# Optimization experiments

Hardware: AMD Instinct MI355X
Metric: run time of the kernel (lower is better)

## Reference

```python
import jax, jax.numpy as jnp
import numpy as np

N = 512       # nodes
V = 8         # n_vectors_hidden
F = 128       # n_invariant_feat_hidden
H = 8         # num_heads
BESSEL = 8
R_MAX = 10.0
FH = F // H
VH = V // H

def _edges(n):
    s, r = np.meshgrid(np.arange(n), np.arange(n), indexing='ij')
    m = s != r
    return jnp.asarray(s[m], jnp.int32), jnp.asarray(r[m], jnp.int32)

def _sph(v):
    # real spherical harmonics ell=1,2,3, e3nn 'component' normalization, unit input v[...,3] -> [...,15]
    x, y, z = v[..., 0], v[..., 1], v[..., 2]
    s3, s15, s5 = np.sqrt(3.0), np.sqrt(15.0), np.sqrt(5.0)
    sh1 = jnp.stack([x, y, z], -1) * s3
    sh2 = jnp.stack([s15 * x * y, s15 * y * z, 0.5 * s5 * (3 * z**2 - 1), s15 * x * z, 0.5 * s15 * (x**2 - y**2)], -1)
    c33, c32, c31, c30 = np.sqrt(35.0 / 8.0), np.sqrt(105.0), np.sqrt(21.0 / 8.0), 0.5 * np.sqrt(7.0)
    sh3 = jnp.stack([c33 * y * (3 * x**2 - y**2), c32 * x * y * z, c31 * y * (5 * z**2 - 1), c30 * z * (5 * z**2 - 3), c31 * x * (5 * z**2 - 1), 0.5 * c32 * z * (x**2 - y**2), c33 * x * (x**2 - 3 * y**2)], -1)
    return jnp.concatenate([sh1, sh2, sh3], -1)

def _bessel(x, n, x_max):
    # e3nn.bessel basis: sqrt(2/x_max) * sin(k*pi*x/x_max) / x, k=1..n
    x = x[..., None]
    k = jnp.arange(1, n + 1, dtype=x.dtype)
    x_safe = jnp.where(x == 0, 1.0, x)
    return np.sqrt(2.0 / x_max) * jnp.sin(k * jnp.pi * x / x_max) / x_safe

def _sus(x):
    return jnp.where(x > 0, jnp.exp(-1.0 / jnp.where(x > 0, x, 1.0)), 0.0)

def _soft_envelope(x, x_max, a=2.0, v0=1.2):
    return v0 * _sus(a * (1.0 - x / x_max)) / _sus(jnp.asarray(a, x.dtype))

def _forward(positions, features, We0, be0, We1, be1, Wq, Wk, Wek, Wv, Wev, Wg, Wo0, bo0, Wo1, bo1, Wo2, bo2):
    n = positions.shape[0]
    senders, receivers = _edges(n)
    vec = positions[senders] - positions[receivers]               # [E,V,3] gather
    lengths = jnp.sqrt(jnp.sum(vec * vec, -1) + 1e-20)            # safe_norm [E,V]
    unit = vec / lengths[..., None]
    sph = _sph(unit)                                              # [E,V,15]
    radial = _bessel(lengths, BESSEL, R_MAX) * _soft_envelope(lengths, R_MAX)[..., None]  # [E,V,B]
    e_scal = radial.reshape(radial.shape[0], -1)                  # [E, V*B]
    h = jax.nn.silu(e_scal @ We0 + be0)
    h = jax.nn.silu(h @ We1 + be1)                                # edge MLP, output_activation=silu
    E = h.shape[0]
    q = (features @ Wq).reshape(n, H, FH)
    k = (features[senders] @ Wk + h @ Wek).reshape(E, H, FH)
    logits = jnp.einsum('ehf,ehf->eh', q[receivers], k) / np.sqrt(FH)
    seg_max = jax.ops.segment_max(logits, receivers, num_segments=n)
    ex = jnp.exp(logits - seg_max[receivers])                     # edge_weight_cutoff = 1
    denom = jax.ops.segment_sum(ex, receivers, num_segments=n)
    alpha = ex / denom[receivers]                                 # [E,H] per-receiver softmax
    v_s = (features[senders] @ Wv + h @ Wev).reshape(E, H, FH)
    gate = h @ Wg                                                 # [E,V] invariant gates
    v_vec = (gate[..., None] * sph[..., :3]).reshape(E, H, VH, 3) # equivariant values from ell=1 sph
    agg_s = jax.ops.segment_sum(alpha[..., None] * v_s, receivers, num_segments=n).reshape(n, F)
    agg_v = jax.ops.segment_sum(alpha[:, :, None, None] * v_vec, receivers, num_segments=n).reshape(n, V, 3)
    o = jax.nn.silu(agg_s @ Wo0 + bo0)
    o = jax.nn.silu(o @ Wo1 + bo1)
    o = o @ Wo2 + bo2                                             # hk MLP: last layer linear
    return (positions + agg_v, features + o)

def setup_inputs() -> dict:
    key = jax.random.key(0)
    ks = jax.random.split(key, 16)
    def w(k, i, o):
        return jax.random.normal(k, (i, o), jnp.float32) / np.sqrt(i)
    M = 128
    D = V * BESSEL
    return {
        'positions': jax.random.normal(ks[0], (N, V, 3), jnp.float32),
        'features': jax.random.normal(ks[1], (N, F), jnp.float32),
        'We0': w(ks[2], D, M), 'be0': jnp.zeros((M,), jnp.float32),
        'We1': w(ks[3], M, M), 'be1': jnp.zeros((M,), jnp.float32),
        'Wq': w(ks[4], F, F), 'Wk': w(ks[5], F, F), 'Wek': w(ks[6], M, F),
        'Wv': w(ks[7], F, F), 'Wev': w(ks[8], M, F), 'Wg': w(ks[9], M, V),
        'Wo0': w(ks[10], F, M), 'bo0': jnp.zeros((M,), jnp.float32),
        'Wo1': w(ks[11], M, M), 'bo1': jnp.zeros((M,), jnp.float32),
        'Wo2': w(ks[12], M, F), 'bo2': jnp.zeros((F,), jnp.float32),
    }

def reference(positions, features, We0, be0, We1, be1, Wq, Wk, Wek, Wv, Wev, Wg, Wo0, bo0, Wo1, bo1, Wo2, bo2):
    return _forward(positions, features, We0, be0, We1, be1, Wq, Wk, Wek, Wv, Wev, Wg, Wo0, bo0, Wo1, bo1, Wo2, bo2)
```

## Files before the change

kernel.cpp:

```cpp
#include <hip/hip_runtime.h>
#include <hip/hip_bf16.h>

#define WS_KNB  0
#define WS_VNT  32768
#define WS_QNB  65536
#define WS_A4T  98304
#define WS_WGT  360448
#define WS_W0T  360960
#define WS_W1T  365056
#define WS_PS   373248
#define PS_STRIDE 1072

typedef short bf16x8 __attribute__((ext_vector_type(8)));
typedef short short4v __attribute__((ext_vector_type(4)));
typedef float f32x4 __attribute__((ext_vector_type(4)));
typedef unsigned short ushort_t;

static __device__ __forceinline__ ushort_t f2b(float x) {
  __hip_bfloat16 h = __float2bfloat16(x);
  return reinterpret_cast<ushort_t&>(h);
}
static __device__ __forceinline__ float b2f(ushort_t u) {
  unsigned v = ((unsigned)u) << 16;
  return reinterpret_cast<float&>(v);
}
static __device__ __forceinline__ float fsilu(float x) {
  return x * __builtin_amdgcn_rcpf(1.f + __expf(-x));
}

static __device__ __forceinline__ bf16x8 radial_frag(
    float dx, float dy, float dz, float& ux, float& uy, float& uz)
{
  const float l2 = fmaf(dx,dx, fmaf(dy,dy, fmaf(dz,dz, 1e-20f)));
  const float inv = rsqrtf(l2);
  const float len = l2 * inv;
  ux = dx*inv; uy = dy*inv; uz = dz*inv;
  const float yy = 2.f - len*0.2f;
  const float env = (yy > 0.f) ? 1.9784655648f * __expf(-__builtin_amdgcn_rcpf(yy)) : 0.f;
  const float coef = 0.4472135955f * env * inv;
  const float arg = len * 0.31415926535f;
  const float s1v = __sinf(arg), c1v = __cosf(arg);
  const float twc = 2.f*c1v;
  float sp = 0.f, sc = s1v;
  bf16x8 ev;
#pragma unroll
  for (int bb = 0; bb < 8; ++bb) {
    ev[bb] = (short)f2b(coef*sc);
    const float nx = fmaf(twc, sc, -sp);
    sp = sc; sc = nx;
  }
  return ev;
}

__global__ __launch_bounds__(128) void k_prep(
    const float* __restrict__ feat, const float* __restrict__ Wq,
    const float* __restrict__ Wk, const float* __restrict__ Wv,
    const float* __restrict__ Wek, const float* __restrict__ Wg,
    const float* __restrict__ We0, const float* __restrict__ We1,
    float* __restrict__ ws)
{
  const int blk = blockIdx.x, j = threadIdx.x;
  if (blk >= 512) {
    const int i = (blk - 512)*128 + j;
    ushort_t* W0T = (ushort_t*)(ws + WS_W0T);
    ushort_t* W1T = (ushort_t*)(ws + WS_W1T);
    if (i < 8192) {
      const int n = i >> 6, k = i & 63;
      W0T[n*64 + k] = f2b(We0[k*128 + n]);
    } else {
      const int t = i - 8192, n = t >> 7, k = t & 127;
      W1T[n*128 + k] = f2b(We1[k*128 + n]);
    }
    return;
  }
  const int r = blk;
  __shared__ float fr[128];
  __shared__ float qL[128];
  fr[j] = feat[r*128 + j];
  __syncthreads();
  float aq = 0.f, ak = 0.f, av = 0.f;
#pragma unroll 4
  for (int i = 0; i < 128; ++i) {
    const float f = fr[i];
    aq = fmaf(f, Wq[i*128 + j], aq);
    ak = fmaf(f, Wk[i*128 + j], ak);
    av = fmaf(f, Wv[i*128 + j], av);
  }
  ushort_t* knB = (ushort_t*)(ws + WS_KNB);
  ushort_t* vnT = (ushort_t*)(ws + WS_VNT);
  ushort_t* qnB = (ushort_t*)(ws + WS_QNB);
  knB[r*128 + j] = f2b(ak);
  vnT[j*512 + r] = f2b(av);
  qnB[r*128 + j] = f2b(0.25f * aq);
  qL[j] = aq;
  __syncthreads();
  ushort_t* A4 = (ushort_t*)(ws + WS_A4T) + r*1024;
  const float* wr = Wek + j*128;
#pragma unroll
  for (int h = 0; h < 8; ++h) {
    float acc = 0.f;
#pragma unroll
    for (int f = 0; f < 16; ++f)
      acc = fmaf(wr[16*h + f], qL[16*h + f], acc);
    A4[h*128 + j] = f2b(acc * 0.25f);
  }
  if (r == 0) {
    ushort_t* WgT = (ushort_t*)(ws + WS_WGT);
#pragma unroll
    for (int v = 0; v < 8; ++v)
      WgT[v*128 + j] = f2b(Wg[j*8 + v]);
  }
}

#define MFMA(a,b,c) __builtin_amdgcn_mfma_f32_16x16x32_bf16((a),(b),(c),0,0,0)

__global__ __launch_bounds__(512, 4) void k_edge14(
    const float* __restrict__ pos,
    const float* __restrict__ be0, const float* __restrict__ be1,
    float* __restrict__ ws)
{
  __shared__ __align__(16) char Lds[40960];
  ushort_t* H1   = (ushort_t*)(Lds);
  ushort_t* Pb   = (ushort_t*)(Lds);
  float*    rscL = (float*)(Lds + 2048);
  ushort_t* H2t  = (ushort_t*)(Lds + 16384);
  ushort_t* Es   = (ushort_t*)(Lds + 32768);
  float*    lgT0 = (float*)(Lds + 32768);
  float*    lgT1 = (float*)(Lds + 36864);

  const int tid = threadIdx.x;
  const int nw = tid >> 6, l = tid & 63;
  const int c = l & 15, g = l >> 4;
  const int b = blockIdx.x;
  const int r = b >> 2, quarter = b & 3;
  const int base = quarter * 128;

  const ushort_t* knB = (const ushort_t*)(ws + WS_KNB);
  const ushort_t* vnT = (const ushort_t*)(ws + WS_VNT);
  const ushort_t* qnB = (const ushort_t*)(ws + WS_QNB);
  const ushort_t* A4G = (const ushort_t*)(ws + WS_A4T) + r*1024;
  const ushort_t* WgG = (const ushort_t*)(ws + WS_WGT);
  const ushort_t* W0T = (const ushort_t*)(ws + WS_W0T);
  const ushort_t* W1T = (const ushort_t*)(ws + WS_W1T);

  const int ncol = nw*16 + c;
  const float be0v = be0[ncol], be1v = be1[ncol];
  const int m_lg = nw & 3, kh = nw >> 2;
  const int ncswz = ((ncol & 7) ^ ((ncol >> 3) & 7)) & 7;

  const float prx = pos[r*24 + nw*3 + 0];
  const float pry = pos[r*24 + nw*3 + 1];
  const float prz = pos[r*24 + nw*3 + 2];

  f32x4 bh = {0,0,0,0}, sna = {0,0,0,0};
  float avx = 0.f, avy = 0.f, avz = 0.f;
  float mrun = -1e30f, drun = 0.f;
  float ux, uy, uz;

  {
    const int sg = base + l;
    const bf16x8 ev = radial_frag(pos[sg*24 + nw*3 + 0] - prx,
                                  pos[sg*24 + nw*3 + 1] - pry,
                                  pos[sg*24 + nw*3 + 2] - prz, ux, uy, uz);
    *(bf16x8*)(Es + l*64 + ((nw ^ (l&7))<<3)) = ev;
  }
  __syncthreads();

  for (int tile = 0; tile < 2; ++tile) {
    const int gbase = base + tile*64;

    float npx = 0.f, npy = 0.f, npz = 0.f;
    if (tile < 1) {
      const int sg = gbase + 64 + l;
      npx = pos[sg*24 + nw*3 + 0];
      npy = pos[sg*24 + nw*3 + 1];
      npz = pos[sg*24 + nw*3 + 2];
    }

    {
      const bf16x8 w0f0 = *(const bf16x8*)(W0T + ncol*64 + g*8);
      const bf16x8 w0f1 = *(const bf16x8*)(W0T + ncol*64 + 32 + g*8);
#pragma unroll
      for (int m = 0; m < 4; ++m) {
        const int ra = m*16 + c;
        const bf16x8 e0 = *(const bf16x8*)(Es + ra*64 + (((g  ) ^ (ra&7))<<3));
        const bf16x8 e1 = *(const bf16x8*)(Es + ra*64 + (((4+g) ^ (ra&7))<<3));
        f32x4 acc = {0,0,0,0};
        acc = MFMA(e0, w0f0, acc);
        acc = MFMA(e1, w0f1, acc);
#pragma unroll
        for (int i = 0; i < 4; ++i) {
          const int row = m*16 + g*4 + i;
          H1[row*128 + (((ncol>>3) ^ (row&15))<<3) + (c&7)] =
              f2b(fsilu(acc[i] + be0v));
        }
      }
    }
    __syncthreads();

#pragma unroll
    for (int m = 0; m < 4; ++m) {
      const int ra = m*16 + c;
      f32x4 acc = {0,0,0,0};
#pragma unroll
      for (int kb = 0; kb < 4; ++kb) {
        const bf16x8 af = *(const bf16x8*)(H1 + ra*128 + (((kb*4+g) ^ (ra&15))<<3));
        const bf16x8 wf = *(const bf16x8*)(W1T + ncol*128 + kb*32 + g*8);
        acc = MFMA(af, wf, acc);
      }
      short4v pk;
#pragma unroll
      for (int i = 0; i < 4; ++i)
        pk[i] = (short)f2b(fsilu(acc[i] + be1v));
      *(short4v*)(H2t + ncol*64 +
          ((((m*2 + (g>>1)) ^ ncswz) & 7)<<3) + (g&1)*4) = pk;
    }
    __syncthreads();

    {
      f32x4 lg = {0,0,0,0};
      if (kh == 0) {
        const int rb = m_lg*2 + (c>>3);
        const int rl = c & 7;
        const ushort_t* ab = (c < 8) ? (A4G + c*128) : (WgG + (c-8)*128);
#pragma unroll
        for (int kb = 0; kb < 4; ++kb) {
          const int cc = (kb*4 + g) & 7;
          bf16x8 bb;
#pragma unroll
          for (int j = 0; j < 8; ++j)
            bb[j] = (short)H2t[(kb*32 + g*8 + j)*64 +
                               (((rb ^ j ^ cc) & 7)<<3) + rl];
          const bf16x8 aw = *(const bf16x8*)(ab + kb*32 + g*8);
          lg = MFMA(aw, bb, lg);
        }
      } else {
        const int srow = gbase + m_lg*16 + c;
#pragma unroll
        for (int kb = 0; kb < 4; ++kb) {
          const bf16x8 bb = *(const bf16x8*)(knB + srow*128 + kb*32 + g*8);
          const bf16x8 qf = *(const bf16x8*)(qnB + r*128 + kb*32 + g*8);
          bf16x8 aw;
          const bool hit = (kb*2 + (g>>1)) == c;
#pragma unroll
          for (int j = 0; j < 8; ++j) aw[j] = hit ? qf[j] : (short)0;
          lg = MFMA(aw, bb, lg);
        }
      }
      float* lgW = kh ? lgT1 : lgT0;
#pragma unroll
      for (int i = 0; i < 4; ++i) {
        const int ch = g*4 + i;
        lgW[ch*64 + ((m_lg*16 + c) ^ (g<<4))] = lg[i];
      }
    }
    __syncthreads();

    {
      const int h = nw;
      const int kv = (h>>2)<<4;
      const int kg = ((8+h)>>2)<<4;
      float lgv = lgT0[h*64 + (l ^ kv)] + lgT1[h*64 + (l ^ kv)];
      const float gate = lgT0[(8+h)*64 + (l ^ kg)] + lgT1[(8+h)*64 + (l ^ kg)];
      if (gbase + l == r) lgv = -1e30f;
      float t = lgv;
      t = fmaxf(t, __shfl_xor(t, 1));
      t = fmaxf(t, __shfl_xor(t, 2));
      t = fmaxf(t, __shfl_xor(t, 4));
      t = fmaxf(t, __shfl_xor(t, 8));
      t = fmaxf(t, __shfl_xor(t, 16));
      t = fmaxf(t, __shfl_xor(t, 32));
      const float mnew = fmaxf(mrun, t);
      const float rsc = __expf(mrun - mnew);
      mrun = mnew;
      const float val = __expf(lgv - mnew);
      float wsm = val;
      wsm += __shfl_xor(wsm, 1);
      wsm += __shfl_xor(wsm, 2);
      wsm += __shfl_xor(wsm, 4);
      wsm += __shfl_xor(wsm, 8);
      wsm += __shfl_xor(wsm, 16);
      wsm += __shfl_xor(wsm, 32);
      drun = drun*rsc + wsm;
      const float ga = val * gate;
      Pb[h*64 + (((l>>3) ^ h)<<3) + (l&7)] = f2b(val);
      Pb[(8+h)*64 + (((l>>3) ^ h)<<3) + (l&7)] = f2b(ga);
      if (l == 0) rscL[h] = rsc;
      avx = avx*rsc + ga*ux;
      avy = avy*rsc + ga*uy;
      avz = avz*rsc + ga*uz;
    }
    __syncthreads();

    {
      float rs[4];
#pragma unroll
      for (int i = 0; i < 4; ++i) rs[i] = rscL[(4*g + i) & 7];
#pragma unroll
      for (int i = 0; i < 4; ++i) { bh[i] *= rs[i]; sna[i] *= rs[i]; }
      const bf16x8 pa0 = *(const bf16x8*)(Pb + c*64 + (((g  ) ^ (c&7))<<3));
      const bf16x8 pa1 = *(const bf16x8*)(Pb + c*64 + (((4+g) ^ (c&7))<<3));
      bh = MFMA(pa0, *(const bf16x8*)(H2t + ncol*64 +
               ((((g  ) ^ ncswz) & 7)<<3)), bh);
      bh = MFMA(pa1, *(const bf16x8*)(H2t + ncol*64 +
               ((((4+g) ^ ncswz) & 7)<<3)), bh);
      const bf16x8 vnf0 = *(const bf16x8*)(vnT + ncol*512 + gbase + g*8);
      const bf16x8 vnf1 = *(const bf16x8*)(vnT + ncol*512 + gbase + 32 + g*8);
      sna = MFMA(pa0, vnf0, sna);
      sna = MFMA(pa1, vnf1, sna);
    }
    if (tile < 1) {
      const bf16x8 ev = radial_frag(npx - prx, npy - pry, npz - prz, ux, uy, uz);
      *(bf16x8*)(Es + l*64 + ((nw ^ (l&7))<<3)) = ev;
      __syncthreads();
    }
  }

  float* PSf = ws + WS_PS + b*PS_STRIDE;
  ushort_t* PSs = (ushort_t*)PSf;
  if (g < 2) {
#pragma unroll
    for (int i = 0; i < 4; ++i) {
      PSs[(4*g + i)*128 + ncol] = f2b(bh[i]);
      PSs[1024 + (4*g + i)*128 + ncol] = f2b(sna[i]);
    }
  }
  avx += __shfl_xor(avx, 1); avy += __shfl_xor(avy, 1); avz += __shfl_xor(avz, 1);
  avx += __shfl_xor(avx, 2); avy += __shfl_xor(avy, 2); avz += __shfl_xor(avz, 2);
  avx += __shfl_xor(avx, 4); avy += __shfl_xor(avy, 4); avz += __shfl_xor(avz, 4);
  avx += __shfl_xor(avx, 8); avy += __shfl_xor(avy, 8); avz += __shfl_xor(avz, 8);
  avx += __shfl_xor(avx,16); avy += __shfl_xor(avy,16); avz += __shfl_xor(avz,16);
  avx += __shfl_xor(avx,32); avy += __shfl_xor(avy,32); avz += __shfl_xor(avz,32);
  if (l == 0) {
    PSf[1024 + nw*3 + 0] = avx;
    PSf[1024 + nw*3 + 1] = avy;
    PSf[1024 + nw*3 + 2] = avz;
    PSf[1048 + nw] = mrun;
    PSf[1056 + nw] = drun;
  }
}

__global__ __launch_bounds__(128) void k_merge(
    const float* __restrict__ pos, const float* __restrict__ feat,
    const float* __restrict__ Wev,
    const float* __restrict__ Wo0, const float* __restrict__ bo0,
    const float* __restrict__ Wo1, const float* __restrict__ bo1,
    const float* __restrict__ Wo2, const float* __restrict__ bo2,
    const float* __restrict__ ws, float* __restrict__ out)
{
  const int r = blockIdx.x, j = threadIdx.x;
  __shared__ float Ss[32], Dh[8];
  __shared__ float BhC[1024];
  __shared__ float asB[128], o1[128], o2[128];
  const float* Pf[4];
  const ushort_t* Ps[4];
#pragma unroll
  for (int i = 0; i < 4; ++i) {
    Pf[i] = ws + WS_PS + (4*r + i)*PS_STRIDE;
    Ps[i] = (const ushort_t*)Pf[i];
  }
  if (j < 8) {
    float M = -1e30f;
#pragma unroll
    for (int i = 0; i < 4; ++i) M = fmaxf(M, Pf[i][1048 + j]);
    float D = 0.f;
#pragma unroll
    for (int i = 0; i < 4; ++i) {
      const float s = __expf(Pf[i][1048 + j] - M);
      Ss[i*8 + j] = s;
      D = fmaf(s, Pf[i][1056 + j], D);
    }
    Dh[j] = D;
  }
  __syncthreads();
#pragma unroll
  for (int h = 0; h < 8; ++h) {
    float acc = 0.f;
#pragma unroll
    for (int i = 0; i < 4; ++i)
      acc = fmaf(Ss[i*8 + h], b2f(Ps[i][h*128 + j]), acc);
    BhC[h*128 + j] = acc;
  }
  const int hh = j >> 4;
  float snj = 0.f;
#pragma unroll
  for (int i = 0; i < 4; ++i)
    snj = fmaf(Ss[i*8 + hh], b2f(Ps[i][1024 + hh*128 + j]), snj);
  if (j < 24) {
    const int v = j / 3;
    float avc = 0.f;
#pragma unroll
    for (int i = 0; i < 4; ++i)
      avc = fmaf(Ss[i*8 + v], Pf[i][1024 + j], avc);
    out[r*24 + j] = pos[r*24 + j]
        + 1.7320508076f * avc * __builtin_amdgcn_rcpf(Dh[v]);
  }
  __syncthreads();
  {
    float ev = 0.f;
#pragma unroll 4
    for (int m = 0; m < 128; ++m)
      ev = fmaf(BhC[hh*128 + m], Wev[m*128 + j], ev);
    asB[j] = (snj + ev) * __builtin_amdgcn_rcpf(Dh[hh]);
  }
  __syncthreads();
  {
    float acc = bo0[j];
#pragma unroll 4
    for (int i = 0; i < 128; ++i) acc = fmaf(asB[i], Wo0[i*128 + j], acc);
    o1[j] = fsilu(acc);
  }
  __syncthreads();
  {
    float acc = bo1[j];
#pragma unroll 4
    for (int i = 0; i < 128; ++i) acc = fmaf(o1[i], Wo1[i*128 + j], acc);
    o2[j] = fsilu(acc);
  }
  __syncthreads();
  {
    float acc = bo2[j];
#pragma unroll 4
    for (int i = 0; i < 128; ++i) acc = fmaf(o2[i], Wo2[i*128 + j], acc);
    out[12288 + r*128 + j] = feat[r*128 + j] + acc;
  }
}

extern "C" void kernel_launch(void* const* d_in, const int* in_sizes, int n_in,
                              void* d_out, int out_size, void* d_ws, size_t ws_size,
                              hipStream_t stream)
{
  const float* pos  = (const float*)d_in[0];
  const float* feat = (const float*)d_in[1];
  const float* We0  = (const float*)d_in[2];
  const float* be0  = (const float*)d_in[3];
  const float* We1  = (const float*)d_in[4];
  const float* be1  = (const float*)d_in[5];
  const float* Wq   = (const float*)d_in[6];
  const float* Wk   = (const float*)d_in[7];
  const float* Wek  = (const float*)d_in[8];
  const float* Wv   = (const float*)d_in[9];
  const float* Wev  = (const float*)d_in[10];
  const float* Wg   = (const float*)d_in[11];
  const float* Wo0  = (const float*)d_in[12];
  const float* bo0  = (const float*)d_in[13];
  const float* Wo1  = (const float*)d_in[14];
  const float* bo1  = (const float*)d_in[15];
  const float* Wo2  = (const float*)d_in[16];
  const float* bo2  = (const float*)d_in[17];
  float* ws  = (float*)d_ws;
  float* out = (float*)d_out;

  hipLaunchKernelGGL(k_prep, dim3(704), dim3(128), 0, stream,
                     feat, Wq, Wk, Wv, Wek, Wg, We0, We1, ws);
  hipLaunchKernelGGL(k_edge14, dim3(2048), dim3(512), 0, stream,
                     pos, be0, be1, ws);
  hipLaunchKernelGGL(k_merge, dim3(512), dim3(128), 0, stream,
                     pos, feat, Wev, Wo0, bo0, Wo1, bo1, Wo2, bo2, ws, out);
}
```

Before: 101.7 us.

## Restructure edge kernel to 256 threads with 32-edge tiles and two columns per lane

The edge kernel drops from 512 to 256 threads per block. Each wave now computes two 16-column output strips, and the edge loop processes four 32-edge tiles instead of two 64-edge tiles, which shrinks LDS from 40 KB to about 25 KB. Weight fragments (W0, the attention/gate A operands, the masked q fragments) are hoisted out of the tile loop, k fragments are prefetched earlier, and bf16 conversions use packed two-at-a-time stores. The aim is higher occupancy and less redundant global loading, at the cost of more barriers per block, smaller MFMA batches and higher register pressure.

```diff
diff --git a/kernel.cpp b/kernel.cpp
--- a/kernel.cpp
+++ b/kernel.cpp
@@ -19,6 +19,10 @@
 static __device__ __forceinline__ ushort_t f2b(float x) {
   __hip_bfloat16 h = __float2bfloat16(x);
   return reinterpret_cast<ushort_t&>(h);
+}
+static __device__ __forceinline__ unsigned pk2(float a, float b) {
+  __hip_bfloat162 t = __float22bfloat162_rn(make_float2(a, b));
+  return reinterpret_cast<unsigned&>(t);
 }
 static __device__ __forceinline__ float b2f(ushort_t u) {
   unsigned v = ((unsigned)u) << 16;
@@ -42,14 +46,17 @@
   const float s1v = __sinf(arg), c1v = __cosf(arg);
   const float twc = 2.f*c1v;
   float sp = 0.f, sc = s1v;
-  bf16x8 ev;
+  float e[8];
 #pragma unroll
   for (int bb = 0; bb < 8; ++bb) {
-    ev[bb] = (short)f2b(coef*sc);
+    e[bb] = coef*sc;
     const float nx = fmaf(twc, sc, -sp);
     sp = sc; sc = nx;
   }
-  return ev;
+  union { bf16x8 v8; unsigned u4[4]; } pk;
+#pragma unroll
+  for (int q = 0; q < 4; ++q) pk.u4[q] = pk2(e[2*q], e[2*q+1]);
+  return pk.v8;
 }
 
 __global__ __launch_bounds__(128) void k_prep(
@@ -114,19 +121,19 @@
 
 #define MFMA(a,b,c) __builtin_amdgcn_mfma_f32_16x16x32_bf16((a),(b),(c),0,0,0)
 
-__global__ __launch_bounds__(512, 4) void k_edge14(
+__global__ __launch_bounds__(256) void k_edge16(
     const float* __restrict__ pos,
     const float* __restrict__ be0, const float* __restrict__ be1,
     float* __restrict__ ws)
 {
-  __shared__ __align__(16) char Lds[40960];
+  __shared__ __align__(16) char Lds[25632];
   ushort_t* H1   = (ushort_t*)(Lds);
-  ushort_t* Pb   = (ushort_t*)(Lds);
-  float*    rscL = (float*)(Lds + 2048);
-  ushort_t* H2t  = (ushort_t*)(Lds + 16384);
-  ushort_t* Es   = (ushort_t*)(Lds + 32768);
-  float*    lgT0 = (float*)(Lds + 32768);
-  float*    lgT1 = (float*)(Lds + 36864);
+  ushort_t* H2t  = (ushort_t*)(Lds + 8192);
+  ushort_t* Es   = (ushort_t*)(Lds + 16384);
+  float*    lgT0 = (float*)(Lds + 20480);
+  float*    lgT1 = (float*)(Lds + 22528);
+  ushort_t* Pb   = (ushort_t*)(Lds + 24576);
+  float*    rscL = (float*)(Lds + 25600);
 
   const int tid = threadIdx.x;
   const int nw = tid >> 6, l = tid & 63;
@@ -143,133 +150,151 @@
   const ushort_t* W0T = (const ushort_t*)(ws + WS_W0T);
   const ushort_t* W1T = (const ushort_t*)(ws + WS_W1T);
 
-  const int ncol = nw*16 + c;
-  const float be0v = be0[ncol], be1v = be1[ncol];
-  const int m_lg = nw & 3, kh = nw >> 2;
-  const int ncswz = ((ncol & 7) ^ ((ncol >> 3) & 7)) & 7;
-
-  const float prx = pos[r*24 + nw*3 + 0];
-  const float pry = pos[r*24 + nw*3 + 1];
-  const float prz = pos[r*24 + nw*3 + 2];
-
-  f32x4 bh = {0,0,0,0}, sna = {0,0,0,0};
+  const int ncol0 = nw*32 + c, ncol1 = nw*32 + 16 + c;
+  const float be00 = be0[ncol0], be01 = be0[ncol1];
+  const float be10 = be1[ncol0], be11 = be1[ncol1];
+  const int csw0 = ((ncol0 & 3) ^ ((ncol0 >> 2) & 3)) & 3;
+  const int csw1 = ((ncol1 & 3) ^ ((ncol1 >> 2) & 3)) & 3;
+  const int m_lg = nw & 1, kh = nw >> 1;
+
+  const bf16x8 w0f00 = *(const bf16x8*)(W0T + ncol0*64 + g*8);
+  const bf16x8 w0f01 = *(const bf16x8*)(W0T + ncol0*64 + 32 + g*8);
+  const bf16x8 w0f10 = *(const bf16x8*)(W0T + ncol1*64 + g*8);
+  const bf16x8 w0f11 = *(const bf16x8*)(W0T + ncol1*64 + 32 + g*8);
+  bf16x8 awf[4];
+  if (kh == 0) {
+    const ushort_t* ab = (c < 8) ? (A4G + c*128) : (WgG + (c-8)*128);
+#pragma unroll
+    for (int kb = 0; kb < 4; ++kb)
+      awf[kb] = *(const bf16x8*)(ab + kb*32 + g*8);
+  } else {
+#pragma unroll
+    for (int kb = 0; kb < 4; ++kb) {
+      const bf16x8 qf = *(const bf16x8*)(qnB + r*128 + kb*32 + g*8);
+      const bool hit = (kb*2 + (g>>1)) == c;
+#pragma unroll
+      for (int j = 0; j < 8; ++j) awf[kb][j] = hit ? qf[j] : (short)0;
+    }
+  }
+
+  const int gsl = l & 31, gv = nw*2 + (l >> 5);
+  const float prx = pos[r*24 + gv*3 + 0];
+  const float pry = pos[r*24 + gv*3 + 1];
+  const float prz = pos[r*24 + gv*3 + 2];
+
+  f32x4 bh0 = {0,0,0,0}, bh1 = {0,0,0,0};
+  f32x4 sn0 = {0,0,0,0}, sn1 = {0,0,0,0};
   float avx = 0.f, avy = 0.f, avz = 0.f;
   float mrun = -1e30f, drun = 0.f;
   float ux, uy, uz;
 
   {
-    const int sg = base + l;
-    const bf16x8 ev = radial_frag(pos[sg*24 + nw*3 + 0] - prx,
-                                  pos[sg*24 + nw*3 + 1] - pry,
-                                  pos[sg*24 + nw*3 + 2] - prz, ux, uy, uz);
-    *(bf16x8*)(Es + l*64 + ((nw ^ (l&7))<<3)) = ev;
-  }
-  __syncthreads();
-
-  for (int tile = 0; tile < 2; ++tile) {
-    const int gbase = base + tile*64;
+    const int sg = base + gsl;
+    const bf16x8 ev = radial_frag(pos[sg*24 + gv*3 + 0] - prx,
+                                  pos[sg*24 + gv*3 + 1] - pry,
+                                  pos[sg*24 + gv*3 + 2] - prz, ux, uy, uz);
+    *(bf16x8*)(Es + gsl*64 + ((gv ^ (gsl&7))<<3)) = ev;
+  }
+  __syncthreads();
+
+  for (int tile = 0; tile < 4; ++tile) {
+    const int gbase = base + tile*32;
 
     float npx = 0.f, npy = 0.f, npz = 0.f;
-    if (tile < 1) {
-      const int sg = gbase + 64 + l;
-      npx = pos[sg*24 + nw*3 + 0];
-      npy = pos[sg*24 + nw*3 + 1];
-      npz = pos[sg*24 + nw*3 + 2];
-    }
-
-    {
-      const bf16x8 w0f0 = *(const bf16x8*)(W0T + ncol*64 + g*8);
-      const bf16x8 w0f1 = *(const bf16x8*)(W0T + ncol*64 + 32 + g*8);
-#pragma unroll
-      for (int m = 0; m < 4; ++m) {
-        const int ra = m*16 + c;
-        const bf16x8 e0 = *(const bf16x8*)(Es + ra*64 + (((g  ) ^ (ra&7))<<3));
-        const bf16x8 e1 = *(const bf16x8*)(Es + ra*64 + (((4+g) ^ (ra&7))<<3));
-        f32x4 acc = {0,0,0,0};
-        acc = MFMA(e0, w0f0, acc);
-        acc = MFMA(e1, w0f1, acc);
-#pragma unroll
-        for (int i = 0; i < 4; ++i) {
-          const int row = m*16 + g*4 + i;
-          H1[row*128 + (((ncol>>3) ^ (row&15))<<3) + (c&7)] =
-              f2b(fsilu(acc[i] + be0v));
-        }
+    if (tile < 3) {
+      const int sg = gbase + 32 + gsl;
+      npx = pos[sg*24 + gv*3 + 0];
+      npy = pos[sg*24 + gv*3 + 1];
+      npz = pos[sg*24 + gv*3 + 2];
+    }
+
+#pragma unroll
+    for (int m = 0; m < 2; ++m) {
+      const int ra = m*16 + c;
+      const bf16x8 e0 = *(const bf16x8*)(Es + ra*64 + (((g  ) ^ (ra&7))<<3));
+      const bf16x8 e1 = *(const bf16x8*)(Es + ra*64 + (((4+g) ^ (ra&7))<<3));
+      f32x4 a0 = {0,0,0,0}, a1 = {0,0,0,0};
+      a0 = MFMA(e0, w0f00, a0); a0 = MFMA(e1, w0f01, a0);
+      a1 = MFMA(e0, w0f10, a1); a1 = MFMA(e1, w0f11, a1);
+#pragma unroll
+      for (int i = 0; i < 4; ++i) {
+        const int row = m*16 + g*4 + i;
+        H1[row*128 + (((ncol0>>3) ^ (row&15))<<3) + (c&7)] = f2b(fsilu(a0[i] + be00));
+        H1[row*128 + (((ncol1>>3) ^ (row&15))<<3) + (c&7)] = f2b(fsilu(a1[i] + be01));
       }
     }
     __syncthreads();
 
-#pragma unroll
-    for (int m = 0; m < 4; ++m) {
+    bf16x8 knf[4];
+    if (kh == 1) {
+      const int srow = gbase + m_lg*16 + c;
+#pragma unroll
+      for (int kb = 0; kb < 4; ++kb)
+        knf[kb] = *(const bf16x8*)(knB + srow*128 + kb*32 + g*8);
+    }
+#pragma unroll
+    for (int m = 0; m < 2; ++m) {
       const int ra = m*16 + c;
-      f32x4 acc = {0,0,0,0};
+      bf16x8 af[4];
+#pragma unroll
+      for (int kb = 0; kb < 4; ++kb)
+        af[kb] = *(const bf16x8*)(H1 + ra*128 + (((kb*4+g) ^ (ra&15))<<3));
+      f32x4 a0 = {0,0,0,0}, a1 = {0,0,0,0};
 #pragma unroll
       for (int kb = 0; kb < 4; ++kb) {
-        const bf16x8 af = *(const bf16x8*)(H1 + ra*128 + (((kb*4+g) ^ (ra&15))<<3));
-        const bf16x8 wf = *(const bf16x8*)(W1T + ncol*128 + kb*32 + g*8);
-        acc = MFMA(af, wf, acc);
+        a0 = MFMA(af[kb], *(const bf16x8*)(W1T + ncol0*128 + kb*32 + g*8), a0);
+        a1 = MFMA(af[kb], *(const bf16x8*)(W1T + ncol1*128 + kb*32 + g*8), a1);
       }
-      short4v pk;
-#pragma unroll
-      for (int i = 0; i < 4; ++i)
-        pk[i] = (short)f2b(fsilu(acc[i] + be1v));
-      *(short4v*)(H2t + ncol*64 +
-          ((((m*2 + (g>>1)) ^ ncswz) & 7)<<3) + (g&1)*4) = pk;
+      const int chnk = m*2 + (g>>1);
+      union { short4v v4; unsigned u2[2]; } p0, p1;
+      p0.u2[0] = pk2(fsilu(a0[0] + be10), fsilu(a0[1] + be10));
+      p0.u2[1] = pk2(fsilu(a0[2] + be10), fsilu(a0[3] + be10));
+      p1.u2[0] = pk2(fsilu(a1[0] + be11), fsilu(a1[1] + be11));
+      p1.u2[1] = pk2(fsilu(a1[2] + be11), fsilu(a1[3] + be11));
+      *(short4v*)(H2t + ncol0*32 + (((chnk ^ csw0) & 3)<<3) + (g&1)*4) = p0.v4;
+      *(short4v*)(H2t + ncol1*32 + (((chnk ^ csw1) & 3)<<3) + (g&1)*4) = p1.v4;
     }
     __syncthreads();
 
     {
       f32x4 lg = {0,0,0,0};
       if (kh == 0) {
-        const int rb = m_lg*2 + (c>>3);
-        const int rl = c & 7;
-        const ushort_t* ab = (c < 8) ? (A4G + c*128) : (WgG + (c-8)*128);
+        const int sb = m_lg*2 + (c>>3);
+        const int si = c & 7;
 #pragma unroll
         for (int kb = 0; kb < 4; ++kb) {
-          const int cc = (kb*4 + g) & 7;
           bf16x8 bb;
 #pragma unroll
-          for (int j = 0; j < 8; ++j)
-            bb[j] = (short)H2t[(kb*32 + g*8 + j)*64 +
-                               (((rb ^ j ^ cc) & 7)<<3) + rl];
-          const bf16x8 aw = *(const bf16x8*)(ab + kb*32 + g*8);
-          lg = MFMA(aw, bb, lg);
+          for (int j = 0; j < 8; ++j) {
+            const int f = kb*32 + g*8 + j;
+            bb[j] = (short)H2t[f*32 + (((sb ^ (f&3) ^ ((f>>2)&3)) & 3)<<3) + si];
+          }
+          lg = MFMA(awf[kb], bb, lg);
         }
       } else {
-        const int srow = gbase + m_lg*16 + c;
-#pragma unroll
-        for (int kb = 0; kb < 4; ++kb) {
-          const bf16x8 bb = *(const bf16x8*)(knB + srow*128 + kb*32 + g*8);
-          const bf16x8 qf = *(const bf16x8*)(qnB + r*128 + kb*32 + g*8);
-          bf16x8 aw;
-          const bool hit = (kb*2 + (g>>1)) == c;
-#pragma unroll
-          for (int j = 0; j < 8; ++j) aw[j] = hit ? qf[j] : (short)0;
-          lg = MFMA(aw, bb, lg);
-        }
+#pragma unroll
+        for (int kb = 0; kb < 4; ++kb)
+          lg = MFMA(awf[kb], knf[kb], lg);
       }
       float* lgW = kh ? lgT1 : lgT0;
 #pragma unroll
-      for (int i = 0; i < 4; ++i) {
-        const int ch = g*4 + i;
-        lgW[ch*64 + ((m_lg*16 + c) ^ (g<<4))] = lg[i];
-      }
+      for (int i = 0; i < 4; ++i)
+        lgW[(g*4 + i)*32 + m_lg*16 + c] = lg[i];
     }
     __syncthreads();
 
     {
-      const int h = nw;
-      const int kv = (h>>2)<<4;
-      const int kg = ((8+h)>>2)<<4;
-      float lgv = lgT0[h*64 + (l ^ kv)] + lgT1[h*64 + (l ^ kv)];
-      const float gate = lgT0[(8+h)*64 + (l ^ kg)] + lgT1[(8+h)*64 + (l ^ kg)];
-      if (gbase + l == r) lgv = -1e30f;
+      const int h = gv;
+      const int sl = gsl;
+      float lgv = lgT0[h*32 + sl] + lgT1[h*32 + sl];
+      const float gate = lgT0[(8+h)*32 + sl] + lgT1[(8+h)*32 + sl];
+      if (gbase + sl == r) lgv = -1e30f;
       float t = lgv;
       t = fmaxf(t, __shfl_xor(t, 1));
       t = fmaxf(t, __shfl_xor(t, 2));
       t = fmaxf(t, __shfl_xor(t, 4));
       t = fmaxf(t, __shfl_xor(t, 8));
       t = fmaxf(t, __shfl_xor(t, 16));
-      t = fmaxf(t, __shfl_xor(t, 32));
       const float mnew = fmaxf(mrun, t);
       const float rsc = __expf(mrun - mnew);
       mrun = mnew;
@@ -280,12 +305,11 @@
       wsm += __shfl_xor(wsm, 4);
       wsm += __shfl_xor(wsm, 8);
       wsm += __shfl_xor(wsm, 16);
-      wsm += __shfl_xor(wsm, 32);
       drun = drun*rsc + wsm;
       const float ga = val * gate;
-      Pb[h*64 + (((l>>3) ^ h)<<3) + (l&7)] = f2b(val);
-      Pb[(8+h)*64 + (((l>>3) ^ h)<<3) + (l&7)] = f2b(ga);
-      if (l == 0) rscL[h] = rsc;
+      Pb[h*32 + ((((sl>>3) ^ (h&3)) & 3)<<3) + (sl&7)] = f2b(val);
+      Pb[(8+h)*32 + ((((sl>>3) ^ ((8+h)&3)) & 3)<<3) + (sl&7)] = f2b(ga);
+      if (sl == 0) rscL[h] = rsc;
       avx = avx*rsc + ga*ux;
       avy = avy*rsc + ga*uy;
       avz = avz*rsc + ga*uz;
@@ -297,21 +321,19 @@
 #pragma unroll
       for (int i = 0; i < 4; ++i) rs[i] = rscL[(4*g + i) & 7];
 #pragma unroll
-      for (int i = 0; i < 4; ++i) { bh[i] *= rs[i]; sna[i] *= rs[i]; }
-      const bf16x8 pa0 = *(const bf16x8*)(Pb + c*64 + (((g  ) ^ (c&7))<<3));
-      const bf16x8 pa1 = *(const bf16x8*)(Pb + c*64 + (((4+g) ^ (c&7))<<3));
-      bh = MFMA(pa0, *(const bf16x8*)(H2t + ncol*64 +
-               ((((g  ) ^ ncswz) & 7)<<3)), bh);
-      bh = MFMA(pa1, *(const bf16x8*)(H2t + ncol*64 +
-               ((((4+g) ^ ncswz) & 7)<<3)), bh);
-      const bf16x8 vnf0 = *(const bf16x8*)(vnT + ncol*512 + gbase + g*8);
-      const bf16x8 vnf1 = *(const bf16x8*)(vnT + ncol*512 + gbase + 32 + g*8);
-      sna = MFMA(pa0, vnf0, sna);
-      sna = MFMA(pa1, vnf1, sna);
-    }
-    if (tile < 1) {
+      for (int i = 0; i < 4; ++i) {
+        bh0[i] *= rs[i]; bh1[i] *= rs[i];
+        sn0[i] *= rs[i]; sn1[i] *= rs[i];
+      }
+      const bf16x8 pa = *(const bf16x8*)(Pb + c*32 + (((g ^ (c&3)) & 3)<<3));
+      bh0 = MFMA(pa, *(const bf16x8*)(H2t + ncol0*32 + (((g ^ csw0) & 3)<<3)), bh0);
+      bh1 = MFMA(pa, *(const bf16x8*)(H2t + ncol1*32 + (((g ^ csw1) & 3)<<3)), bh1);
+      sn0 = MFMA(pa, *(const bf16x8*)(vnT + ncol0*512 + gbase + g*8), sn0);
+      sn1 = MFMA(pa, *(const bf16x8*)(vnT + ncol1*512 + gbase + g*8), sn1);
+    }
+    if (tile < 3) {
       const bf16x8 ev = radial_frag(npx - prx, npy - pry, npz - prz, ux, uy, uz);
-      *(bf16x8*)(Es + l*64 + ((nw ^ (l&7))<<3)) = ev;
+      *(bf16x8*)(Es + gsl*64 + ((gv ^ (gsl&7))<<3)) = ev;
       __syncthreads();
     }
   }
@@ -321,8 +343,10 @@
   if (g < 2) {
 #pragma unroll
     for (int i = 0; i < 4; ++i) {
-      PSs[(4*g + i)*128 + ncol] = f2b(bh[i]);
-      PSs[1024 + (4*g + i)*128 + ncol] = f2b(sna[i]);
+      PSs[(4*g + i)*128 + ncol0] = f2b(bh0[i]);
+      PSs[(4*g + i)*128 + ncol1] = f2b(bh1[i]);
+      PSs[1024 + (4*g + i)*128 + ncol0] = f2b(sn0[i]);
+      PSs[1024 + (4*g + i)*128 + ncol1] = f2b(sn1[i]);
     }
   }
   avx += __shfl_xor(avx, 1); avy += __shfl_xor(avy, 1); avz += __shfl_xor(avz, 1);
@@ -330,13 +354,12 @@
   avx += __shfl_xor(avx, 4); avy += __shfl_xor(avy, 4); avz += __shfl_xor(avz, 4);
   avx += __shfl_xor(avx, 8); avy += __shfl_xor(avy, 8); avz += __shfl_xor(avz, 8);
   avx += __shfl_xor(avx,16); avy += __shfl_xor(avy,16); avz += __shfl_xor(avz,16);
-  avx += __shfl_xor(avx,32); avy += __shfl_xor(avy,32); avz += __shfl_xor(avz,32);
-  if (l == 0) {
-    PSf[1024 + nw*3 + 0] = avx;
-    PSf[1024 + nw*3 + 1] = avy;
-    PSf[1024 + nw*3 + 2] = avz;
-    PSf[1048 + nw] = mrun;
-    PSf[1056 + nw] = drun;
+  if (gsl == 0) {
+    PSf[1024 + gv*3 + 0] = avx;
+    PSf[1024 + gv*3 + 1] = avy;
+    PSf[1024 + gv*3 + 2] = avz;
+    PSf[1048 + gv] = mrun;
+    PSf[1056 + gv] = drun;
   }
 }
 
@@ -453,7 +476,7 @@
 
   hipLaunchKernelGGL(k_prep, dim3(704), dim3(128), 0, stream,
                      feat, Wq, Wk, Wv, Wek, Wg, We0, We1, ws);
-  hipLaunchKernelGGL(k_edge14, dim3(2048), dim3(512), 0, stream,
+  hipLaunchKernelGGL(k_edge16, dim3(2048), dim3(256), 0, stream,
                      pos, be0, be1, ws);
   hipLaunchKernelGGL(k_merge, dim3(512), dim3(128), 0, stream,
                      pos, feat, Wev, Wo0, bo0, Wo1, bo1, Wo2, bo2, ws, out);
```

Result: slower. 111.9 us (+10.0%).
